# Optimization experiments

Hardware: AMD Instinct MI355X
Metric: run time of the kernel (lower is better)

The kernel has to match this reference:

```python
import math
import jax, jax.numpy as jnp
import numpy as np

N_HEADS = 16
D_KV = 64
NUM_BUCKETS = 32
MAX_DISTANCE = 128


def _relative_position_bucket(relative_position, num_buckets=NUM_BUCKETS, max_distance=MAX_DISTANCE):
    # bidirectional=True (encoder)
    num_buckets //= 2
    n = -relative_position
    ret = (n < 0).astype(jnp.int32) * num_buckets
    n = jnp.abs(n)
    max_exact = num_buckets // 2
    is_small = n < max_exact
    val_if_large = max_exact + (
        jnp.log(jnp.maximum(n, 1).astype(jnp.float32) / max_exact)
        / math.log(max_distance / max_exact)
        * (num_buckets - max_exact)
    ).astype(jnp.int32)
    val_if_large = jnp.minimum(val_if_large, num_buckets - 1)
    return ret + jnp.where(is_small, n, val_if_large)


def setup_inputs() -> dict:
    key = jax.random.key(0)
    ks = jax.random.split(key, 6)
    B, S, D = 2, 2048, 1024
    scale = 0.02  # keep pre-softmax logits in a sane range
    return {
        "x": jax.random.normal(ks[0], (B, S, D), dtype=jnp.float32),
        "Wq": jax.random.normal(ks[1], (D, N_HEADS * D_KV), dtype=jnp.float32) * scale,
        "Wk": jax.random.normal(ks[2], (D, N_HEADS * D_KV), dtype=jnp.float32) * scale,
        "Wv": jax.random.normal(ks[3], (D, N_HEADS * D_KV), dtype=jnp.float32) * scale,
        "Wo": jax.random.normal(ks[4], (N_HEADS * D_KV, D), dtype=jnp.float32) * scale,
        "rel_emb": jax.random.normal(ks[5], (NUM_BUCKETS, N_HEADS), dtype=jnp.float32) * scale,
    }


def reference(x, Wq, Wk, Wv, Wo, rel_emb):
    B, S, D = x.shape
    H, Dk = N_HEADS, D_KV

    def shape(t):  # [B,S,H*Dk] -> [B,H,S,Dk]
        return t.reshape(B, S, H, Dk).transpose(0, 2, 1, 3)

    q = shape(x @ Wq)
    k = shape(x @ Wk)
    v = shape(x @ Wv)

    # NOTE: T5 attention has NO 1/sqrt(d) scaling.
    scores = jnp.einsum("bhqd,bhkd->bhqk", q, k)

    # relative position bias: [1, H, S, S]
    ctx_pos = jnp.arange(S)[:, None]
    mem_pos = jnp.arange(S)[None, :]
    rp_bucket = _relative_position_bucket(mem_pos - ctx_pos)  # [S, S]
    position_bias = rel_emb[rp_bucket].transpose(2, 0, 1)[None]  # [1,H,S,S]

    weights = jax.nn.softmax(scores + position_bias, axis=-1)
    context = jnp.einsum("bhqk,bhkd->bhqd", weights, v)
    context = context.transpose(0, 2, 1, 3).reshape(B, S, H * Dk)
    return context @ Wo
```

## Files before the change

kernel.cpp:

```cpp
#include <hip/hip_runtime.h>
#include <math.h>

typedef unsigned short u16;
typedef unsigned int u32;
typedef __attribute__((ext_vector_type(8))) short bf16x8_t;
typedef __attribute__((ext_vector_type(4))) float f32x4_t;

#define S_LEN  2048
#define NH     16
#define DK     64
#define DMODEL 1024
#define MROWS  4096
#define LOG2E  1.44269504088896f

__device__ inline u16 f2b(float f) {
  union { float f; u32 u; } c; c.f = f;
  u32 u = c.u;
  return (u16)((u + 0x7fffu + ((u >> 16) & 1u)) >> 16);
}

__device__ __forceinline__ float fexp2(float x) {
#if __has_builtin(__builtin_amdgcn_exp2f)
  return __builtin_amdgcn_exp2f(x);
#else
  return exp2f(x);
#endif
}

__device__ __forceinline__ void stage16(const u16* gp_lane, u16* lds_base) {
#if __has_builtin(__builtin_amdgcn_global_load_lds)
  __builtin_amdgcn_global_load_lds((const __attribute__((address_space(1))) u32*)gp_lane,
                                   (__attribute__((address_space(3))) u32*)lds_base, 16, 0, 0);
#else
  *(uint4*)(lds_base + (threadIdx.x & 63) * 8) = *(const uint4*)gp_lane;
#endif
}

__global__ void prep_kernel(const float* __restrict__ x,
                            const float* __restrict__ Wq, const float* __restrict__ Wk,
                            const float* __restrict__ Wv, const float* __restrict__ Wo,
                            const float* __restrict__ rel,
                            u16* __restrict__ xb, u16* __restrict__ Wall,
                            u16* __restrict__ Wto, float* __restrict__ btab) {
  __shared__ float tile[32][33];
  const int bid = blockIdx.x, t = threadIdx.x;
  if (bid < 4096) {
    int i = (bid * 256 + t) * 4;
    float4 v = *(const float4*)(x + i);
    ushort4 o;
    o.x = f2b(v.x); o.y = f2b(v.y); o.z = f2b(v.z); o.w = f2b(v.w);
    *(ushort4*)(xb + i) = o;
  } else if (bid < 8192) {
    int bid2 = bid - 4096;
    int z = bid2 >> 10, rem = bid2 & 1023;
    const float* W; u16* Wt;
    switch (z) {
      case 0: W = Wq; Wt = Wall; break;
      case 1: W = Wk; Wt = Wall + (size_t)DMODEL * DMODEL; break;
      case 2: W = Wv; Wt = Wall + (size_t)2 * DMODEL * DMODEL; break;
      default: W = Wo; Wt = Wto; break;
    }
    int bc = (rem & 31) * 32, br = (rem >> 5) * 32;
    int tx = t & 31, ty = t >> 5;
    #pragma unroll
    for (int yy = 0; yy < 32; yy += 8)
      tile[ty + yy][tx] = W[(size_t)(br + ty + yy) * DMODEL + bc + tx];
    __syncthreads();
    #pragma unroll
    for (int yy = 0; yy < 32; yy += 8)
      Wt[(size_t)(bc + ty + yy) * DMODEL + br + tx] = f2b(tile[tx][ty + yy]);
  } else {
    int idx = (bid - 8192) * 256 + t;
    if (idx < NH * 4095) {
      int h = idx / 4095;
      int dpos = idx - h * 4095;
      int delta = dpos - 2047;
      int ret = (delta > 0) ? 16 : 0;
      int n = delta < 0 ? -delta : delta;
      int bucket;
      if (n < 8) {
        bucket = ret + n;
      } else {
        float vf = logf((float)n * 0.125f) / 2.7725887222397811f * 8.0f;
        int vil = 8 + (int)vf;
        bucket = ret + (vil < 15 ? vil : 15);
      }
      btab[idx] = (rel[bucket * NH + h] - 16.0f) * LOG2E;
    }
  }
}

#define GSTR 56
template <int MODE>
__global__ __launch_bounds__(256) void gemm128_kernel(const u16* __restrict__ A,
                                                      const u16* __restrict__ Bt,
                                                      float* __restrict__ C,
                                                      u16* __restrict__ q16,
                                                      u16* __restrict__ k16,
                                                      u16* __restrict__ vt16) {
  constexpr int ABSZ = (MODE == 1) ? 4608 : 128 * GSTR;
  constexpr int FSTR = (MODE == 1) ? 32 : GSTR;
  __shared__ __align__(16) u16 As[ABSZ];
  __shared__ __align__(16) u16 Bs[ABSZ];
  const int t = threadIdx.x, w = t >> 6, l = t & 63;
  const int c = l & 15, quad = l >> 4;
  const int m0 = blockIdx.x * 128, n0 = blockIdx.y * 128;
  const int wm = (w & 1) * 64, wn = (w >> 1) * 64;

  f32x4_t acc[16] = {};

  if constexpr (MODE == 1) {
    const int sr = l >> 2;
    const int k8 = (l & 3) * 8;
    const u16* Ag0 = A  + (size_t)(m0 + w * 32 + sr) * DMODEL + k8;
    const u16* Ag1 = Ag0 + (size_t)16 * DMODEL;
    const u16* Bg0 = Bt + (size_t)(n0 + w * 32 + sr) * DMODEL + k8;
    const u16* Bg1 = Bg0 + (size_t)16 * DMODEL;
    u16* Al = As + w * 1024;
    u16* Bl = Bs + w * 1024;
    for (int k0 = 0; k0 < DMODEL; k0 += 32) {
      __syncthreads();
      stage16(Ag0 + k0, Al);
      stage16(Ag1 + k0, Al + 512);
      stage16(Bg0 + k0, Bl);
      stage16(Bg1 + k0, Bl + 512);
      __syncthreads();
      bf16x8_t af[4], bfr[4];
      #pragma unroll
      for (int i = 0; i < 4; ++i) {
        af[i]  = *(const bf16x8_t*)(As + (wm + i * 16 + c) * FSTR + quad * 8);
        bfr[i] = *(const bf16x8_t*)(Bs + (wn + i * 16 + c) * FSTR + quad * 8);
      }
      #pragma unroll
      for (int mt = 0; mt < 4; ++mt)
        #pragma unroll
        for (int nt = 0; nt < 4; ++nt)
          acc[mt * 4 + nt] = __builtin_amdgcn_mfma_f32_16x16x32_bf16(af[mt], bfr[nt], acc[mt * 4 + nt], 0, 0, 0);
    }
  } else {
    const int sr = t >> 2;
    const int k8 = (t & 3) * 8;
    const u16* Ag0 = A  + (size_t)(m0 + sr) * DMODEL + k8;
    const u16* Ag1 = Ag0 + (size_t)64 * DMODEL;
    const u16* Bg0 = Bt + (size_t)(n0 + sr) * DMODEL + k8;
    const u16* Bg1 = Bg0 + (size_t)64 * DMODEL;
    u16* Al0 = As + sr * GSTR + k8;
    u16* Al1 = Al0 + 64 * GSTR;
    u16* Bl0 = Bs + sr * GSTR + k8;
    u16* Bl1 = Bl0 + 64 * GSTR;

    uint4 a0 = *(const uint4*)Ag0, a1 = *(const uint4*)Ag1;
    uint4 b0 = *(const uint4*)Bg0, b1 = *(const uint4*)Bg1;
    for (int k0 = 0; k0 < DMODEL; k0 += 32) {
      __syncthreads();
      *(uint4*)Al0 = a0; *(uint4*)Al1 = a1;
      *(uint4*)Bl0 = b0; *(uint4*)Bl1 = b1;
      __syncthreads();
      if (k0 + 32 < DMODEL) {
        a0 = *(const uint4*)(Ag0 + k0 + 32);
        a1 = *(const uint4*)(Ag1 + k0 + 32);
        b0 = *(const uint4*)(Bg0 + k0 + 32);
        b1 = *(const uint4*)(Bg1 + k0 + 32);
      }
      bf16x8_t af[4], bfr[4];
      #pragma unroll
      for (int i = 0; i < 4; ++i) {
        af[i]  = *(const bf16x8_t*)(As + (wm + i * 16 + c) * FSTR + quad * 8);
        bfr[i] = *(const bf16x8_t*)(Bs + (wn + i * 16 + c) * FSTR + quad * 8);
      }
      #pragma unroll
      for (int mt = 0; mt < 4; ++mt)
        #pragma unroll
        for (int nt = 0; nt < 4; ++nt)
          acc[mt * 4 + nt] = __builtin_amdgcn_mfma_f32_16x16x32_bf16(af[mt], bfr[nt], acc[mt * 4 + nt], 0, 0, 0);
    }
  }

  if constexpr (MODE == 0) {
    #pragma unroll
    for (int mt = 0; mt < 4; ++mt) {
      int grow0 = m0 + wm + mt * 16 + quad * 4;
      #pragma unroll
      for (int nt = 0; nt < 4; ++nt) {
        int gcol = n0 + wn + nt * 16 + c;
        #pragma unroll
        for (int r = 0; r < 4; ++r)
          C[(size_t)(grow0 + r) * DMODEL + gcol] = acc[mt * 4 + nt][r];
      }
    }
  } else {
    const int whichblk = n0 >> 10;
    if (whichblk == 2) {
      #pragma unroll
      for (int mt = 0; mt < 4; ++mt) {
        int grow0 = m0 + wm + mt * 16 + quad * 4;
        int b = grow0 >> 11, s0 = grow0 & 2047;
        #pragma unroll
        for (int nt = 0; nt < 4; ++nt) {
          int cc = (n0 + wn + nt * 16 + c) & 1023;
          int hh = cc >> 6, dk = cc & 63;
          f32x4_t v4 = acc[mt * 4 + nt];
          ushort4 o;
          o.x = f2b(v4[0]); o.y = f2b(v4[1]); o.z = f2b(v4[2]); o.w = f2b(v4[3]);
          *(ushort4*)(vt16 + (((size_t)(b * NH + hh)) * DK + dk) * S_LEN + s0) = o;
        }
      }
    } else {
      u16* tb = (w & 1) ? Bs : As;
      const int base_mw = m0 + wm;
      const int bb = base_mw >> 11, s0g = base_mw & 2047;
      const int cc = (n0 + wn) & 1023;
      const int hh = cc >> 6;
      u16* qk = (whichblk == 0 ? q16 : k16) + (((size_t)(bb * NH + hh)) * S_LEN + s0g) * DK;
      __syncthreads();
      #pragma unroll
      for (int round = 0; round < 2; ++round) {
        if ((w >> 1) == round) {
          #pragma unroll
          for (int mt = 0; mt < 4; ++mt)
            #pragma unroll
            for (int nt = 0; nt < 4; ++nt)
              #pragma unroll
              for (int r = 0; r < 4; ++r)
                tb[(mt * 16 + quad * 4 + r) * 72 + nt * 16 + c] = f2b(acc[mt * 4 + nt][r]);
          #pragma unroll
          for (int i = 0; i < 8; ++i) {
            int lrow = i * 8 + (l >> 3);
            int chk = l & 7;
            uint4 vv = *(const uint4*)(tb + lrow * 72 + chk * 8);
            *(uint4*)(qk + (size_t)lrow * DK + chk * 8) = vv;
          }
        }
        __syncthreads();
      }
    }
  }
}

#define ASTR 72
__global__ __launch_bounds__(512, 4) void attn_mfma_kernel(const u16* __restrict__ q,
                                                           const u16* __restrict__ k,
                                                           const u16* __restrict__ vt,
                                                           const float* __restrict__ btab,
                                                           u16* __restrict__ ctx) {
  __shared__ __align__(16) u16 Ks[64 * ASTR];
  __shared__ __align__(16) u16 Vts[64 * ASTR];
  __shared__ __align__(16) u16 Ps[8][16 * ASTR];
  __shared__ float band[192];

  const int t = threadIdx.x;
  const int w = t >> 6, l = t & 63;
  const int c = l & 15, quad = l >> 4;
  const int bh = blockIdx.y;
  const int h = bh & (NH - 1), b = bh >> 4;
  const int q0 = blockIdx.x * 128;

  const u16* qb = q + (size_t)bh * S_LEN * DK;
  const u16* kb = k + (size_t)bh * S_LEN * DK;
  const u16* vb = vt + (size_t)bh * DK * S_LEN;
  const float* btp = btab + h * 4095 + (2047 - 127 - q0);

  bf16x8_t qfrag[2];
  {
    const u16* qp = qb + (size_t)(q0 + w * 16 + c) * DK + quad * 8;
    qfrag[0] = *(const bf16x8_t*)(qp);
    qfrag[1] = *(const bf16x8_t*)(qp + 32);
  }

  float lp = 0.f;
  f32x4_t O[4] = {};

  const int srow = t >> 3;
  const int sc8 = (t & 7) * 8;
  const u16* kg = kb + (size_t)srow * DK + sc8;
  const u16* vg = vb + (size_t)srow * S_LEN + sc8;
  u16* Kl = Ks + srow * ASTR + sc8;
  u16* Vl = Vts + srow * ASTR + sc8;
  u16* Pw = Ps[w];
  const int qit = w * 16 + c;

  uint4 kr = *(const uint4*)kg;
  uint4 vr = *(const uint4*)vg;
  float br = (t < 192) ? btp[t] : 0.f;

  for (int kt = 0; kt < S_LEN; kt += 64) {
    const int D = kt - q0;
    const bool far = (D >= 256) || (D <= -192);
    *(uint4*)Kl = kr;
    *(uint4*)Vl = vr;
    if (t < 192) band[t] = br;
    __syncthreads();
    if (kt + 64 < S_LEN) {
      kr = *(const uint4*)(kg + (size_t)(kt + 64) * DK);
      vr = *(const uint4*)(vg + (kt + 64));
      br = (t < 192) ? btp[kt + 64 + t] : 0.f;
    }

    f32x4_t s4[4] = {};
    #pragma unroll
    for (int kc = 0; kc < 2; ++kc) {
      bf16x8_t kf[4];
      #pragma unroll
      for (int nt = 0; nt < 4; ++nt)
        kf[nt] = *(const bf16x8_t*)(Ks + (nt * 16 + c) * ASTR + kc * 32 + quad * 8);
      #pragma unroll
      for (int nt = 0; nt < 4; ++nt)
        s4[nt] = __builtin_amdgcn_mfma_f32_16x16x32_bf16(kf[nt], qfrag[kc], s4[nt], 0, 0, 0);
    }

    if (far) {
      const float bfc = band[127];
      #pragma unroll
      for (int nt = 0; nt < 4; ++nt) {
        float p0 = fexp2(fmaf(s4[nt][0], LOG2E, bfc));
        float p1 = fexp2(fmaf(s4[nt][1], LOG2E, bfc));
        float p2 = fexp2(fmaf(s4[nt][2], LOG2E, bfc));
        float p3 = fexp2(fmaf(s4[nt][3], LOG2E, bfc));
        lp += (p0 + p1) + (p2 + p3);
        u32 w01, w23;
        asm("v_cvt_pk_bf16_f32 %0, %1, %2" : "=v"(w01) : "v"(p0), "v"(p1));
        asm("v_cvt_pk_bf16_f32 %0, %1, %2" : "=v"(w23) : "v"(p2), "v"(p3));
        *(u32*)(Pw + c * ASTR + nt * 16 + quad * 4)     = w01;
        *(u32*)(Pw + c * ASTR + nt * 16 + quad * 4 + 2) = w23;
      }
    } else {
      const int bnd0 = 127 + quad * 4 - qit;
      #pragma unroll
      for (int nt = 0; nt < 4; ++nt) {
        float p0 = fexp2(fmaf(s4[nt][0], LOG2E, band[bnd0 + nt * 16 + 0]));
        float p1 = fexp2(fmaf(s4[nt][1], LOG2E, band[bnd0 + nt * 16 + 1]));
        float p2 = fexp2(fmaf(s4[nt][2], LOG2E, band[bnd0 + nt * 16 + 2]));
        float p3 = fexp2(fmaf(s4[nt][3], LOG2E, band[bnd0 + nt * 16 + 3]));
        lp += (p0 + p1) + (p2 + p3);
        u32 w01, w23;
        asm("v_cvt_pk_bf16_f32 %0, %1, %2" : "=v"(w01) : "v"(p0), "v"(p1));
        asm("v_cvt_pk_bf16_f32 %0, %1, %2" : "=v"(w23) : "v"(p2), "v"(p3));
        *(u32*)(Pw + c * ASTR + nt * 16 + quad * 4)     = w01;
        *(u32*)(Pw + c * ASTR + nt * 16 + quad * 4 + 2) = w23;
      }
    }

    #pragma unroll
    for (int kc = 0; kc < 2; ++kc) {
      bf16x8_t afr = *(const bf16x8_t*)(Pw + c * ASTR + kc * 32 + quad * 8);
      #pragma unroll
      for (int nt = 0; nt < 4; ++nt) {
        bf16x8_t vfr = *(const bf16x8_t*)(Vts + (nt * 16 + c) * ASTR + kc * 32 + quad * 8);
        O[nt] = __builtin_amdgcn_mfma_f32_16x16x32_bf16(afr, vfr, O[nt], 0, 0, 0);
      }
    }
    __syncthreads();
  }

  lp += __shfl_xor(lp, 16, 64);
  lp += __shfl_xor(lp, 32, 64);

  #pragma unroll
  for (int r = 0; r < 4; ++r) {
    float inv = 1.0f / __shfl(lp, quad * 4 + r, 64);
    int s = q0 + w * 16 + quad * 4 + r;
    u16* cp = ctx + ((size_t)(b * S_LEN + s)) * DMODEL + h * DK + c;
    #pragma unroll
    for (int nt = 0; nt < 4; ++nt)
      cp[nt * 16] = f2b(O[nt][r] * inv);
  }
}

extern "C" void kernel_launch(void* const* d_in, const int* in_sizes, int n_in,
                              void* d_out, int out_size, void* d_ws, size_t ws_size,
                              hipStream_t stream) {
  const float* x   = (const float*)d_in[0];
  const float* Wq  = (const float*)d_in[1];
  const float* Wk  = (const float*)d_in[2];
  const float* Wv  = (const float*)d_in[3];
  const float* Wo  = (const float*)d_in[4];
  const float* rel = (const float*)d_in[5];
  float* out = (float*)d_out;

  char* ws = (char*)d_ws;
  size_t off = 0;
  auto carve = [&](size_t bytes) -> char* {
    char* p = ws + off;
    off += (bytes + 255) & ~(size_t)255;
    return p;
  };
  u16*   xb   = (u16*)  carve((size_t)MROWS * DMODEL * 2);
  u16*   Wall = (u16*)  carve((size_t)3 * DMODEL * DMODEL * 2);
  u16*   Wto  = (u16*)  carve((size_t)DMODEL * DMODEL * 2);
  u16*   qb16 = (u16*)  carve((size_t)4194304 * 2);
  u16*   kb16 = (u16*)  carve((size_t)4194304 * 2);
  u16*   vt16 = (u16*)  carve((size_t)4194304 * 2);
  float* btab = (float*)carve(((size_t)NH * 4095 + 256) * 4);
  u16*   ctxb = (u16*)  carve((size_t)4194304 * 2);

  prep_kernel<<<8448, 256, 0, stream>>>(x, Wq, Wk, Wv, Wo, rel, xb, Wall, Wto, btab);

  dim3 qkvgrid(32, 24);
  gemm128_kernel<1><<<qkvgrid, 256, 0, stream>>>(xb, Wall, nullptr, qb16, kb16, vt16);

  dim3 agrid(S_LEN / 128, 32);
  attn_mfma_kernel<<<agrid, 512, 0, stream>>>(qb16, kb16, vt16, btab, ctxb);

  dim3 ogrid(32, 8);
  gemm128_kernel<0><<<ogrid, 256, 0, stream>>>(ctxb, Wto, out, nullptr, nullptr, nullptr);
}
```

Baseline: 194.1 us.

## Switch attention to 32x32x16 MFMA with in-register P via permlane swap and split-K waves

Restructures the attention inner loop to use 32x32x16 bf16 MFMA tiles. Each pair of waves shares a 32-query group and splits the 64-key tile in half, and the two halves' partial outputs and row sums are combined through LDS at the end. The softmax probabilities are repacked into MFMA A-operand layout in registers with v_permlane32_swap instead of a round trip through LDS, which removes the per-wave P buffer. s_setprio hints are added around the MFMA sections. The aim is to cut LDS traffic and instruction count, at the cost of a larger LDS reduction buffer that may lower occupancy, and an extra final sync.

```diff
diff --git a/kernel.cpp b/kernel.cpp
--- a/kernel.cpp
+++ b/kernel.cpp
@@ -5,6 +5,7 @@
 typedef unsigned int u32;
 typedef __attribute__((ext_vector_type(8))) short bf16x8_t;
 typedef __attribute__((ext_vector_type(4))) float f32x4_t;
+typedef __attribute__((ext_vector_type(16))) float f32x16_t;
 
 #define S_LEN  2048
 #define NH     16
@@ -25,6 +26,16 @@
 #else
   return exp2f(x);
 #endif
+}
+
+__device__ __forceinline__ u32 cvtpk(float lo, float hi) {
+  u32 r;
+  asm("v_cvt_pk_bf16_f32 %0, %1, %2" : "=v"(r) : "v"(lo), "v"(hi));
+  return r;
+}
+
+__device__ __forceinline__ void plswap(u32 &x, u32 &y) {
+  asm("v_permlane32_swap_b32 %0, %1" : "+v"(x), "+v"(y));
 }
 
 __device__ __forceinline__ void stage16(const u16* gp_lane, u16* lds_base) {
@@ -245,12 +256,14 @@
                                                            u16* __restrict__ ctx) {
   __shared__ __align__(16) u16 Ks[64 * ASTR];
   __shared__ __align__(16) u16 Vts[64 * ASTR];
-  __shared__ __align__(16) u16 Ps[8][16 * ASTR];
   __shared__ float band[192];
+  __shared__ float Ored[4][64][33];
+  __shared__ float lpx[4][32];
 
   const int t = threadIdx.x;
   const int w = t >> 6, l = t & 63;
-  const int c = l & 15, quad = l >> 4;
+  const int c32 = l & 31, h32 = l >> 5;
+  const int grp = w >> 1, kh = w & 1;
   const int bh = blockIdx.y;
   const int h = bh & (NH - 1), b = bh >> 4;
   const int q0 = blockIdx.x * 128;
@@ -260,15 +273,17 @@
   const u16* vb = vt + (size_t)bh * DK * S_LEN;
   const float* btp = btab + h * 4095 + (2047 - 127 - q0);
 
-  bf16x8_t qfrag[2];
+  bf16x8_t qfrag[4];
   {
-    const u16* qp = qb + (size_t)(q0 + w * 16 + c) * DK + quad * 8;
+    const u16* qp = qb + (size_t)(q0 + grp * 32 + c32) * DK + h32 * 8;
     qfrag[0] = *(const bf16x8_t*)(qp);
-    qfrag[1] = *(const bf16x8_t*)(qp + 32);
+    qfrag[1] = *(const bf16x8_t*)(qp + 16);
+    qfrag[2] = *(const bf16x8_t*)(qp + 32);
+    qfrag[3] = *(const bf16x8_t*)(qp + 48);
   }
 
   float lp = 0.f;
-  f32x4_t O[4] = {};
+  f32x16_t O0 = {}, O1 = {};
 
   const int srow = t >> 3;
   const int sc8 = (t & 7) * 8;
@@ -276,12 +291,13 @@
   const u16* vg = vb + (size_t)srow * S_LEN + sc8;
   u16* Kl = Ks + srow * ASTR + sc8;
   u16* Vl = Vts + srow * ASTR + sc8;
-  u16* Pw = Ps[w];
-  const int qit = w * 16 + c;
 
   uint4 kr = *(const uint4*)kg;
   uint4 vr = *(const uint4*)vg;
   float br = (t < 192) ? btp[t] : 0.f;
+
+  const int krow = kh * 32 + c32;
+  const int bndc = 127 + kh * 32 + 4 * h32 - grp * 32 - c32;
 
   for (int kt = 0; kt < S_LEN; kt += 64) {
     const int D = kt - q0;
@@ -296,73 +312,83 @@
       br = (t < 192) ? btp[kt + 64 + t] : 0.f;
     }
 
-    f32x4_t s4[4] = {};
-    #pragma unroll
-    for (int kc = 0; kc < 2; ++kc) {
-      bf16x8_t kf[4];
-      #pragma unroll
-      for (int nt = 0; nt < 4; ++nt)
-        kf[nt] = *(const bf16x8_t*)(Ks + (nt * 16 + c) * ASTR + kc * 32 + quad * 8);
-      #pragma unroll
-      for (int nt = 0; nt < 4; ++nt)
-        s4[nt] = __builtin_amdgcn_mfma_f32_16x16x32_bf16(kf[nt], qfrag[kc], s4[nt], 0, 0, 0);
-    }
-
+    f32x16_t s4 = {};
+    __builtin_amdgcn_s_setprio(1);
+    #pragma unroll
+    for (int kb4 = 0; kb4 < 4; ++kb4) {
+      bf16x8_t kf = *(const bf16x8_t*)(Ks + krow * ASTR + kb4 * 16 + h32 * 8);
+      s4 = __builtin_amdgcn_mfma_f32_32x32x16_bf16(kf, qfrag[kb4], s4, 0, 0, 0);
+    }
+    __builtin_amdgcn_s_setprio(0);
+
+    float p[16];
     if (far) {
       const float bfc = band[127];
       #pragma unroll
-      for (int nt = 0; nt < 4; ++nt) {
-        float p0 = fexp2(fmaf(s4[nt][0], LOG2E, bfc));
-        float p1 = fexp2(fmaf(s4[nt][1], LOG2E, bfc));
-        float p2 = fexp2(fmaf(s4[nt][2], LOG2E, bfc));
-        float p3 = fexp2(fmaf(s4[nt][3], LOG2E, bfc));
-        lp += (p0 + p1) + (p2 + p3);
-        u32 w01, w23;
-        asm("v_cvt_pk_bf16_f32 %0, %1, %2" : "=v"(w01) : "v"(p0), "v"(p1));
-        asm("v_cvt_pk_bf16_f32 %0, %1, %2" : "=v"(w23) : "v"(p2), "v"(p3));
-        *(u32*)(Pw + c * ASTR + nt * 16 + quad * 4)     = w01;
-        *(u32*)(Pw + c * ASTR + nt * 16 + quad * 4 + 2) = w23;
-      }
+      for (int r = 0; r < 16; ++r)
+        p[r] = fexp2(fmaf(s4[r], LOG2E, bfc));
     } else {
-      const int bnd0 = 127 + quad * 4 - qit;
-      #pragma unroll
-      for (int nt = 0; nt < 4; ++nt) {
-        float p0 = fexp2(fmaf(s4[nt][0], LOG2E, band[bnd0 + nt * 16 + 0]));
-        float p1 = fexp2(fmaf(s4[nt][1], LOG2E, band[bnd0 + nt * 16 + 1]));
-        float p2 = fexp2(fmaf(s4[nt][2], LOG2E, band[bnd0 + nt * 16 + 2]));
-        float p3 = fexp2(fmaf(s4[nt][3], LOG2E, band[bnd0 + nt * 16 + 3]));
-        lp += (p0 + p1) + (p2 + p3);
-        u32 w01, w23;
-        asm("v_cvt_pk_bf16_f32 %0, %1, %2" : "=v"(w01) : "v"(p0), "v"(p1));
-        asm("v_cvt_pk_bf16_f32 %0, %1, %2" : "=v"(w23) : "v"(p2), "v"(p3));
-        *(u32*)(Pw + c * ASTR + nt * 16 + quad * 4)     = w01;
-        *(u32*)(Pw + c * ASTR + nt * 16 + quad * 4 + 2) = w23;
-      }
-    }
-
-    #pragma unroll
-    for (int kc = 0; kc < 2; ++kc) {
-      bf16x8_t afr = *(const bf16x8_t*)(Pw + c * ASTR + kc * 32 + quad * 8);
-      #pragma unroll
-      for (int nt = 0; nt < 4; ++nt) {
-        bf16x8_t vfr = *(const bf16x8_t*)(Vts + (nt * 16 + c) * ASTR + kc * 32 + quad * 8);
-        O[nt] = __builtin_amdgcn_mfma_f32_16x16x32_bf16(afr, vfr, O[nt], 0, 0, 0);
-      }
-    }
+      #pragma unroll
+      for (int r = 0; r < 16; ++r)
+        p[r] = fexp2(fmaf(s4[r], LOG2E, band[bndc + (r & 3) + 8 * (r >> 2)]));
+    }
+    #pragma unroll
+    for (int r = 0; r < 16; ++r)
+      lp += p[r];
+
+    union PW { u32 wds[4]; bf16x8_t v; } pa0, pa1;
+    {
+      u32 x, y;
+      x = cvtpk(p[0], p[1]);  y = cvtpk(p[4], p[5]);   plswap(x, y);
+      pa0.wds[0] = x; pa0.wds[2] = y;
+      x = cvtpk(p[2], p[3]);  y = cvtpk(p[6], p[7]);   plswap(x, y);
+      pa0.wds[1] = x; pa0.wds[3] = y;
+      x = cvtpk(p[8], p[9]);  y = cvtpk(p[12], p[13]); plswap(x, y);
+      pa1.wds[0] = x; pa1.wds[2] = y;
+      x = cvtpk(p[10], p[11]); y = cvtpk(p[14], p[15]); plswap(x, y);
+      pa1.wds[1] = x; pa1.wds[3] = y;
+    }
+
+    __builtin_amdgcn_s_setprio(1);
+    {
+      bf16x8_t vf00 = *(const bf16x8_t*)(Vts + (c32)      * ASTR + kh * 32 + h32 * 8);
+      bf16x8_t vf01 = *(const bf16x8_t*)(Vts + (32 + c32) * ASTR + kh * 32 + h32 * 8);
+      O0 = __builtin_amdgcn_mfma_f32_32x32x16_bf16(pa0.v, vf00, O0, 0, 0, 0);
+      O1 = __builtin_amdgcn_mfma_f32_32x32x16_bf16(pa0.v, vf01, O1, 0, 0, 0);
+      bf16x8_t vf10 = *(const bf16x8_t*)(Vts + (c32)      * ASTR + kh * 32 + 16 + h32 * 8);
+      bf16x8_t vf11 = *(const bf16x8_t*)(Vts + (32 + c32) * ASTR + kh * 32 + 16 + h32 * 8);
+      O0 = __builtin_amdgcn_mfma_f32_32x32x16_bf16(pa1.v, vf10, O0, 0, 0, 0);
+      O1 = __builtin_amdgcn_mfma_f32_32x32x16_bf16(pa1.v, vf11, O1, 0, 0, 0);
+    }
+    __builtin_amdgcn_s_setprio(0);
     __syncthreads();
   }
 
-  lp += __shfl_xor(lp, 16, 64);
   lp += __shfl_xor(lp, 32, 64);
 
-  #pragma unroll
-  for (int r = 0; r < 4; ++r) {
-    float inv = 1.0f / __shfl(lp, quad * 4 + r, 64);
-    int s = q0 + w * 16 + quad * 4 + r;
-    u16* cp = ctx + ((size_t)(b * S_LEN + s)) * DMODEL + h * DK + c;
-    #pragma unroll
-    for (int nt = 0; nt < 4; ++nt)
-      cp[nt * 16] = f2b(O[nt][r] * inv);
+  if (kh == 1) {
+    #pragma unroll
+    for (int r = 0; r < 16; ++r) {
+      Ored[grp][l][r]      = O0[r];
+      Ored[grp][l][16 + r] = O1[r];
+    }
+    if (l < 32) lpx[grp][l] = lp;
+  }
+  __syncthreads();
+  if (kh == 0) {
+    lp += lpx[grp][c32];
+    float rv = 1.0f / lp;
+    #pragma unroll
+    for (int r = 0; r < 16; ++r) {
+      int qr = (r & 3) + 8 * (r >> 2) + 4 * h32;
+      float inv = __shfl(rv, qr, 64);
+      float o0 = O0[r] + Ored[grp][l][r];
+      float o1 = O1[r] + Ored[grp][l][16 + r];
+      int s = q0 + grp * 32 + qr;
+      u16* cp = ctx + ((size_t)(b * S_LEN + s)) * DMODEL + h * DK;
+      cp[c32]      = f2b(o0 * inv);
+      cp[32 + c32] = f2b(o1 * inv);
+    }
   }
 }
 
```

Result: faster. 186.1 us (-4.1%).
